# Kernel tuning notes

Measured on AMD Instinct MI355X. Metric: run time of the kernel, lower is better.

The kernel has to match this reference:

```python
import jax, jax.numpy as jnp
import numpy as np

B, S, E, H = 2, 2048, 512, 8
D = E // H
BETA = 0.5
SCALE = float(np.sqrt(D))


def setup_inputs() -> dict:
    key = jax.random.key(0)
    ks = jax.random.split(key, 22)
    inp = {}
    for i, n in enumerate(["qx", "qy", "kx", "ky", "vx", "vy"]):
        inp[n] = jax.random.normal(ks[i], (B, S, E), jnp.float32)
    wnames = ["Wqx", "Wqy", "Wkx", "Wky", "Wvx", "Wvy", "Wox", "Woy"]
    for i, n in enumerate(wnames):
        inp[n] = jax.random.normal(ks[6 + i], (E, E), jnp.float32) * 0.02
        inp["b" + n[1:]] = jnp.zeros((E,), jnp.float32)
    return inp


def _split_heads(x):
    # [B, S, E] -> [B, H, S, D]
    return x.reshape(B, S, H, D).transpose(0, 2, 1, 3)


def _merge_heads(x):
    # [B, H, S, D] -> [B, S, E]
    return x.transpose(0, 2, 1, 3).reshape(B, S, E)


def reference(qx, qy, kx, ky, vx, vy,
              Wqx, bqx, Wqy, bqy, Wkx, bkx, Wky, bky,
              Wvx, bvx, Wvy, bvy, Wox, box, Woy, boy):
    lin = lambda x, W, b: x @ W.T + b  # torch nn.Linear convention
    qxh = _split_heads(lin(qx, Wqx, bqx))
    qyh = _split_heads(lin(qy, Wqy, bqy))
    kxh = _split_heads(lin(kx, Wkx, bkx))
    kyh = _split_heads(lin(ky, Wky, bky))
    vxh = _split_heads(lin(vx, Wvx, bvx))
    vyh = _split_heads(lin(vy, Wvy, bvy))

    # polar decomposition of the bichannel: radius, angle
    aq = jnp.arctan2(qyh, qxh)  # [B,H,S,D]
    ak = jnp.arctan2(kyh, kxh)
    # mean_d cos(aq - ak) == (cos_q @ cos_k^T + sin_q @ sin_k^T) / D
    # (avoids the [B,H,Sq,Sk,D] angle_diff tensor; same math)
    phase = (jnp.einsum('bhqd,bhkd->bhqk', jnp.cos(aq), jnp.cos(ak))
             + jnp.einsum('bhqd,bhkd->bhqk', jnp.sin(aq), jnp.sin(ak))) / D

    rq = jnp.sqrt(qxh * qxh + qyh * qyh)
    rk = jnp.sqrt(kxh * kxh + kyh * kyh)
    mag = jnp.einsum('bhqd,bhkd->bhqk', rq, rk) / SCALE

    scores = BETA * phase + (1.0 - BETA) * mag  # [B,H,Sq,Sk]
    attn = jax.nn.softmax(scores, axis=-1)      # dropout is identity in eval

    ax = _merge_heads(jnp.einsum('bhqk,bhkd->bhqd', attn, vxh))
    ay = _merge_heads(jnp.einsum('bhqk,bhkd->bhqd', attn, vyh))
    return lin(ax, Wox, box), lin(ay, Woy, boy)
```

## Files before the change

kernel.cpp:

```cpp
#include <hip/hip_runtime.h>
#include <hip/hip_bf16.h>


#define N_ROWS 4096
#define EDIM 512
#define SEQ 2048
#define NHEAD 8
#define HDIM 64
#define CDIM 192
#define DV 128

#define PHASE_A 0.08838834764831845f
#define MAG_B   0.25f
#define SM_SHIFT 8.0f

typedef _Float16 half8 __attribute__((ext_vector_type(8)));
typedef float f32x4 __attribute__((ext_vector_type(4)));

__device__ inline void gload16(const void* g, void* l) {
    __builtin_amdgcn_global_load_lds(
        (const __attribute__((address_space(1))) unsigned int*)g,
        (__attribute__((address_space(3))) unsigned int*)l, 16, 0, 0);
}

#define KSW(r) (((((r) & 3) | (((r) >> 1) & 4))) << 4)

struct Cvt14 { const float* s[14]; _Float16* d[14]; int n8[14]; };

__global__ __launch_bounds__(256) void cvt_fp16(Cvt14 j) {
    const float* s = j.s[blockIdx.y];
    _Float16* d = j.d[blockIdx.y];
    const int n8 = j.n8[blockIdx.y];
    union U { _Float16 h[8]; uint4 u; };
    for (int i = blockIdx.x * 256 + threadIdx.x; i < n8; i += gridDim.x * 256) {
        const float4 f0 = ((const float4*)s)[2 * i];
        const float4 f1 = ((const float4*)s)[2 * i + 1];
        U u;
        u.h[0] = (_Float16)f0.x; u.h[1] = (_Float16)f0.y;
        u.h[2] = (_Float16)f0.z; u.h[3] = (_Float16)f0.w;
        u.h[4] = (_Float16)f1.x; u.h[5] = (_Float16)f1.y;
        u.h[6] = (_Float16)f1.z; u.h[7] = (_Float16)f1.w;
        ((uint4*)d)[i] = u.u;
    }
}

struct PairArgs {
    const _Float16* x0; const _Float16* x1;
    const _Float16* w0; const _Float16* w1;
    const float* b0;    const float* b1;
    void* dst0;         void* dst1;
};

template <int FUSED>
__global__ __launch_bounds__(256, 3) void gemm16(PairArgs A0, PairArgs A1, PairArgs A2)
{
    __shared__ _Float16 As0[128 * 32];
    __shared__ _Float16 As1[128 * 32];
    __shared__ _Float16 Bs0[64 * 32];
    __shared__ _Float16 Bs1[64 * 32];

    const int tid = threadIdx.x;
    const int w = tid >> 6, l = tid & 63;
    const int g = l >> 4, ql = l & 15;
    const int wr = w >> 1, wc = w & 1;
    const int z = FUSED ? blockIdx.z : 0;
    const PairArgs& A = FUSED ? (z == 0 ? A0 : (z == 1 ? A1 : A2)) : A0;

    const int m0 = blockIdx.y * 128;
    const int n0 = blockIdx.x * 64;

    f32x4 acc0[4][2], acc1[4][2];
    #pragma unroll
    for (int f = 0; f < 4; ++f)
        #pragma unroll
        for (int e = 0; e < 2; ++e) {
            acc0[f][e] = (f32x4){0.f, 0.f, 0.f, 0.f};
            acc1[f][e] = (f32x4){0.f, 0.f, 0.f, 0.f};
        }

    for (int k0 = 0; k0 < EDIM; k0 += 32) {
        __syncthreads();
        #pragma unroll
        for (int i = 0; i < 2; ++i) {
            const int s = i * 256 + tid;
            const int row = s >> 2, c = s & 3;
            const int cs = c ^ ((row >> 1) & 3);
            gload16(A.x0 + (size_t)(m0 + row) * EDIM + k0 + cs * 8,
                    As0 + (i * 256 + w * 64) * 8);
        }
        #pragma unroll
        for (int i = 0; i < 2; ++i) {
            const int s = i * 256 + tid;
            const int row = s >> 2, c = s & 3;
            const int cs = c ^ ((row >> 1) & 3);
            gload16(A.x1 + (size_t)(m0 + row) * EDIM + k0 + cs * 8,
                    As1 + (i * 256 + w * 64) * 8);
        }
        {
            const int row = tid >> 2, c = tid & 3;
            const int cs = c ^ ((row >> 1) & 3);
            gload16(A.w0 + (size_t)(n0 + row) * EDIM + k0 + cs * 8,
                    Bs0 + (w * 64) * 8);
            gload16(A.w1 + (size_t)(n0 + row) * EDIM + k0 + cs * 8,
                    Bs1 + (w * 64) * 8);
        }
        __syncthreads();

        half8 af0[4], af1[4], bf0[2], bf1[2];
        #pragma unroll
        for (int f = 0; f < 4; ++f) {
            const int arow = wr * 64 + f * 16 + ql;
            const int byo = arow * 64 + ((g ^ ((arow >> 1) & 3)) << 4);
            af0[f] = *(const half8*)((const char*)As0 + byo);
            af1[f] = *(const half8*)((const char*)As1 + byo);
        }
        #pragma unroll
        for (int e = 0; e < 2; ++e) {
            const int brow = wc * 32 + e * 16 + ql;
            const int byo = brow * 64 + ((g ^ ((brow >> 1) & 3)) << 4);
            bf0[e] = *(const half8*)((const char*)Bs0 + byo);
            bf1[e] = *(const half8*)((const char*)Bs1 + byo);
        }
        #pragma unroll
        for (int f = 0; f < 4; ++f)
            #pragma unroll
            for (int e = 0; e < 2; ++e) {
                acc0[f][e] = __builtin_amdgcn_mfma_f32_16x16x32_f16(
                    af0[f], bf0[e], acc0[f][e], 0, 0, 0);
                acc1[f][e] = __builtin_amdgcn_mfma_f32_16x16x32_f16(
                    af1[f], bf1[e], acc1[f][e], 0, 0, 0);
            }
    }

    #pragma unroll
    for (int f = 0; f < 4; ++f) {
        const int mb = m0 + wr * 64 + f * 16 + g * 4;
        #pragma unroll
        for (int e = 0; e < 2; ++e) {
            const int n = n0 + wc * 32 + e * 16 + ql;
            const float bias0 = A.b0[n];
            const float bias1 = A.b1[n];
            if (!FUSED) {
                float* o0 = (float*)A.dst0;
                float* o1 = (float*)A.dst1;
                #pragma unroll
                for (int r = 0; r < 4; ++r) {
                    const int m = mb + r;
                    o0[(size_t)m * EDIM + n] = acc0[f][e][r] + bias0;
                    o1[(size_t)m * EDIM + n] = acc1[f][e][r] + bias1;
                }
            } else {
                const int b = mb >> 11, s = mb & (SEQ - 1);
                const int h = blockIdx.x;
                const int d = n & (HDIM - 1);
                const int bh = b * NHEAD + h;
                _Float16* dst = (_Float16*)A.dst0;
                if (z != 2) {
                    const size_t base = ((size_t)bh * SEQ + s) * CDIM + d;
                    #pragma unroll
                    for (int r = 0; r < 4; ++r) {
                        const float v0 = acc0[f][e][r] + bias0;
                        const float v1 = acc1[f][e][r] + bias1;
                        const float r2 = v0 * v0 + v1 * v1;
                        const float rm = sqrtf(r2);
                        float c, sn;
                        if (r2 > 0.f) { c = v0 / rm; sn = v1 / rm; }
                        else          { c = 1.f;     sn = 0.f; }
                        dst[base + (size_t)r * CDIM]       = (_Float16)(c  * PHASE_A);
                        dst[base + (size_t)r * CDIM + 64]  = (_Float16)(sn * PHASE_A);
                        dst[base + (size_t)r * CDIM + 128] = (_Float16)(rm * MAG_B);
                    }
                } else {
                    union Pk { _Float16 h[4]; uint2 u; } p0, p1;
                    #pragma unroll
                    for (int r = 0; r < 4; ++r) {
                        p0.h[r] = (_Float16)(acc0[f][e][r] + bias0);
                        p1.h[r] = (_Float16)(acc1[f][e][r] + bias1);
                    }
                    *(uint2*)&dst[((size_t)bh * DV + d) * SEQ + s]      = p0.u;
                    *(uint2*)&dst[((size_t)bh * DV + 64 + d) * SEQ + s] = p1.u;
                }
            }
        }
    }
}

__global__ __launch_bounds__(512, 2) void attn_mfma(
    const _Float16* __restrict__ Qg, const _Float16* __restrict__ Kg,
    const _Float16* __restrict__ Vg,
    _Float16* __restrict__ ax, _Float16* __restrict__ ay)
{
    __shared__ char smem[81920];

    const int tid = threadIdx.x;
    const int w  = tid >> 6;
    const int l  = tid & 63;
    const int g  = l >> 4;
    const int ql = l & 15;

    const int d  = blockIdx.x;
    const int xcd = d & 7;
    const int j   = d >> 3;
    const int bh  = xcd + 8 * (j >> 4);
    const int q0  = (j & 15) * 128;
    const int b  = bh >> 3, h = bh & 7;
    const int qrow = q0 + w * 16 + ql;

    half8 qf[6];
    {
        const char* qp = (const char*)(Qg + ((size_t)bh * SEQ + qrow) * CDIM);
        #pragma unroll
        for (int c = 0; c < 6; ++c) {
            uint4 u = *(const uint4*)(qp + c * 64 + g * 16);
            qf[c] = __builtin_bit_cast(half8, u);
        }
    }

    f32x4 o[8];
    #pragma unroll
    for (int vt = 0; vt < 8; ++vt) o[vt] = (f32x4){0.f, 0.f, 0.f, 0.f};
    float l_i = 0.f;

    const char* kgb = (const char*)(Kg + (size_t)bh * SEQ * CDIM);
    const char* vgb = (const char*)(Vg + (size_t)bh * DV * SEQ);

    int koff[3], vofs[2];
    #pragma unroll
    for (int i = 0; i < 3; ++i) {
        const int beta = (w * 3 + i) * 1024 + l * 16;
        const int r = beta / 384;
        const int cb = (beta - r * 384) ^ KSW(r);
        koff[i] = r * 384 + cb;
    }
    #pragma unroll
    for (int i = 0; i < 2; ++i) {
        const int beta = (w * 2 + i) * 1024 + l * 16;
        const int r = beta >> 7;
        const int cb = (beta & 127) ^ ((r & 7) << 4);
        vofs[i] = r * 4096 + cb;
    }

    const int rq = ((ql >> 2) << 3) + (ql & 3);
    const int kxor = ((ql & 3) | (((ql >> 2) & 1) << 2)) << 4;

    #define STAGE(kbase, vbase, kt0)                                          \
        { _Pragma("unroll")                                                   \
          for (int i = 0; i < 3; ++i)                                         \
              gload16(kgb + (size_t)(kt0) * 384 + koff[i],                    \
                      smem + (kbase) + (w * 3 + i) * 1024);                   \
          _Pragma("unroll")                                                   \
          for (int i = 0; i < 2; ++i)                                         \
              gload16(vgb + (size_t)(kt0) * 2 + vofs[i],                      \
                      smem + (vbase) + (w * 2 + i) * 1024); }

    auto COMPUTE = [&](const int kbase, const int vbase) {
        f32x4 st[4];
        __builtin_amdgcn_s_setprio(1);
        #pragma unroll
        for (int kt = 0; kt < 4; ++kt) {
            f32x4 acc = {0.f, 0.f, 0.f, 0.f};
            const int r_p = rq + (kt & 1) * 32 + ((kt >> 1) << 2);
            #pragma unroll
            for (int c = 0; c < 6; ++c) {
                uint4 u = *(const uint4*)(
                    smem + kbase + ((r_p * 384 + c * 64 + g * 16) ^ kxor));
                acc = __builtin_amdgcn_mfma_f32_16x16x32_f16(
                    __builtin_bit_cast(half8, u), qf[c], acc, 0, 0, 0);
            }
            st[kt] = acc;
        }
        __builtin_amdgcn_s_setprio(0);

        float rs = 0.f;
        #pragma unroll
        for (int kt = 0; kt < 4; ++kt)
            #pragma unroll
            for (int r = 0; r < 4; ++r) {
                const float p = __expf(st[kt][r] - SM_SHIFT);
                st[kt][r] = p; rs += p;
            }
        rs += __shfl_xor(rs, 16);
        rs += __shfl_xor(rs, 32);
        l_i += rs;

        half8 pf[2];
        #pragma unroll
        for (int ks = 0; ks < 2; ++ks) {
            union { _Float16 h[8]; half8 v; } u;
            u.h[0] = (_Float16)st[ks][0];     u.h[1] = (_Float16)st[ks][1];
            u.h[2] = (_Float16)st[ks][2];     u.h[3] = (_Float16)st[ks][3];
            u.h[4] = (_Float16)st[ks + 2][0]; u.h[5] = (_Float16)st[ks + 2][1];
            u.h[6] = (_Float16)st[ks + 2][2]; u.h[7] = (_Float16)st[ks + 2][3];
            pf[ks] = u.v;
        }

        __builtin_amdgcn_s_setprio(1);
        #pragma unroll
        for (int vt = 0; vt < 8; ++vt) {
            const int v = vt * 16 + ql;
            uint4 u0 = *(const uint4*)(
                smem + vbase + ((v * 128 + g * 16) ^ ((v & 7) << 4)));
            uint4 u1 = *(const uint4*)(
                smem + vbase + ((v * 128 + 64 + g * 16) ^ ((v & 7) << 4)));
            o[vt] = __builtin_amdgcn_mfma_f32_16x16x32_f16(
                pf[0], __builtin_bit_cast(half8, u0), o[vt], 0, 0, 0);
            o[vt] = __builtin_amdgcn_mfma_f32_16x16x32_f16(
                pf[1], __builtin_bit_cast(half8, u1), o[vt], 0, 0, 0);
        }
        __builtin_amdgcn_s_setprio(0);
    };

    STAGE(0, 49152, 0);
    for (int t = 0; t < 32; t += 2) {
        __syncthreads();
        STAGE(24576, 65536, (t + 1) * 64);
        COMPUTE(0, 49152);
        __syncthreads();
        if (t + 2 < 32) STAGE(0, 49152, (t + 2) * 64);
        COMPUTE(24576, 65536);
    }
    #undef STAGE

    const float invl = 1.f / l_i;
    const float fi0 = __shfl(invl, g * 4 + 0);
    const float fi1 = __shfl(invl, g * 4 + 1);
    const float fi2 = __shfl(invl, g * 4 + 2);
    const float fi3 = __shfl(invl, g * 4 + 3);
    #pragma unroll
    for (int vt = 0; vt < 8; ++vt) {
        const int v = vt * 16 + ql;
        _Float16* basep = (vt < 4) ? ax : ay;
        const int vv = v & 63;
        const float fi[4] = {fi0, fi1, fi2, fi3};
        #pragma unroll
        for (int r = 0; r < 4; ++r) {
            const int q = q0 + w * 16 + g * 4 + r;
            basep[((size_t)(b * SEQ + q)) * EDIM + h * HDIM + vv] =
                (_Float16)(o[vt][r] * fi[r]);
        }
    }
}

extern "C" void kernel_launch(void* const* d_in, const int* in_sizes, int n_in,
                              void* d_out, int out_size, void* d_ws, size_t ws_size,
                              hipStream_t stream)
{
    const float* act[6];
    for (int i = 0; i < 6; ++i) act[i] = (const float*)d_in[i];
    const float* W[8]; const float* Bv[8];
    for (int i = 0; i < 8; ++i) {
        W[i]  = (const float*)d_in[6 + 2 * i];
        Bv[i] = (const float*)d_in[7 + 2 * i];
    }

    float* outx = (float*)d_out;
    float* outy = outx + 2097152;

    _Float16* ws = (_Float16*)d_ws;
    _Float16* act16[6];
    for (int i = 0; i < 6; ++i) act16[i] = ws + (size_t)i * 2097152;
    _Float16* w16[8];
    for (int i = 0; i < 8; ++i) w16[i] = ws + 12582912 + (size_t)i * 262144;
    _Float16* Qt16 = ws + 14680064;
    _Float16* Kt16 = Qt16 + 6291456;
    _Float16* Vt16 = Kt16 + 6291456;
    _Float16* ax16 = Vt16 + 4194304;
    _Float16* ay16 = ax16 + 2097152;

    Cvt14 jc{};
    for (int i = 0; i < 6; ++i) { jc.s[i] = act[i]; jc.d[i] = act16[i]; jc.n8[i] = 262144; }
    for (int i = 0; i < 8; ++i) { jc.s[6 + i] = W[i]; jc.d[6 + i] = w16[i]; jc.n8[6 + i] = 32768; }
    hipLaunchKernelGGL(cvt_fp16, dim3(256, 14), dim3(256), 0, stream, jc);

    PairArgs qa{act16[0], act16[1], w16[0], w16[1], Bv[0], Bv[1], Qt16, nullptr};
    PairArgs ka{act16[2], act16[3], w16[2], w16[3], Bv[2], Bv[3], Kt16, nullptr};
    PairArgs va{act16[4], act16[5], w16[4], w16[5], Bv[4], Bv[5], Vt16, nullptr};
    hipLaunchKernelGGL((gemm16<1>), dim3(8, 32, 3), dim3(256), 0, stream, qa, ka, va);

    hipLaunchKernelGGL(attn_mfma, dim3(256), dim3(512), 0, stream,
                       Qt16, Kt16, Vt16, ax16, ay16);

    PairArgs oa{ax16, ay16, w16[6], w16[7], Bv[6], Bv[7], outx, outy};
    hipLaunchKernelGGL((gemm16<0>), dim3(8, 32, 1), dim3(256), 0, stream, oa, oa, oa);
}
```

Before: 138.0 us.

## Fuse fp32-to-fp16 activation conversion into QKV GEMM and double-buffer LDS

Removes the separate conversion pass over the six fp32 activation tensors. The fused QKV GEMM now loads fp32 activations into registers, converts them to fp16 and writes them to LDS. The GEMM mainloop also becomes double-buffered, prefetching the next K slice while computing the current one, which takes one sync per iteration instead of two. This saves a full read and write of the activation traffic, but the GEMM now reads twice the bytes per activation tile and uses more registers and LDS, which may lower occupancy.

```diff
diff --git a/kernel.cpp b/kernel.cpp
--- a/kernel.cpp
+++ b/kernel.cpp
@@ -25,12 +25,11 @@
 
 #define KSW(r) (((((r) & 3) | (((r) >> 1) & 4))) << 4)
 
-struct Cvt14 { const float* s[14]; _Float16* d[14]; int n8[14]; };
-
-__global__ __launch_bounds__(256) void cvt_fp16(Cvt14 j) {
+struct Cvt8 { const float* s[8]; _Float16* d[8]; };
+
+__global__ __launch_bounds__(256) void cvt_fp16(Cvt8 j, int n8) {
     const float* s = j.s[blockIdx.y];
     _Float16* d = j.d[blockIdx.y];
-    const int n8 = j.n8[blockIdx.y];
     union U { _Float16 h[8]; uint4 u; };
     for (int i = blockIdx.x * 256 + threadIdx.x; i < n8; i += gridDim.x * 256) {
         const float4 f0 = ((const float4*)s)[2 * i];
@@ -45,7 +44,7 @@
 }
 
 struct PairArgs {
-    const _Float16* x0; const _Float16* x1;
+    const void* x0;     const void* x1;
     const _Float16* w0; const _Float16* w1;
     const float* b0;    const float* b1;
     void* dst0;         void* dst1;
@@ -54,10 +53,7 @@
 template <int FUSED>
 __global__ __launch_bounds__(256, 3) void gemm16(PairArgs A0, PairArgs A1, PairArgs A2)
 {
-    __shared__ _Float16 As0[128 * 32];
-    __shared__ _Float16 As1[128 * 32];
-    __shared__ _Float16 Bs0[64 * 32];
-    __shared__ _Float16 Bs1[64 * 32];
+    __shared__ _Float16 smem[2][12288];
 
     const int tid = threadIdx.x;
     const int w = tid >> 6, l = tid & 63;
@@ -69,6 +65,60 @@
     const int m0 = blockIdx.y * 128;
     const int n0 = blockIdx.x * 64;
 
+    size_t srcA[2];
+    #pragma unroll
+    for (int i = 0; i < 2; ++i) {
+        const int s = i * 256 + tid;
+        const int row = s >> 2, c = s & 3;
+        const int cs = c ^ ((row >> 1) & 3);
+        srcA[i] = (size_t)(m0 + row) * EDIM + cs * 8;
+    }
+    const int rowB = tid >> 2;
+    const int csB = (tid & 3) ^ ((rowB >> 1) & 3);
+    const size_t srcB = (size_t)(n0 + rowB) * EDIM + csB * 8;
+
+    const float* x0f = (const float*)A.x0;
+    const float* x1f = (const float*)A.x1;
+    const _Float16* x0h = (const _Float16*)A.x0;
+    const _Float16* x1h = (const _Float16*)A.x1;
+
+    float4 xr[2][2][2];
+
+    #define LOADX(k0)                                                         \
+        do { _Pragma("unroll")                                                \
+          for (int i = 0; i < 2; ++i) {                                       \
+              const float* p0 = x0f + srcA[i] + (k0);                         \
+              const float* p1 = x1f + srcA[i] + (k0);                         \
+              xr[0][i][0] = *(const float4*)p0;                               \
+              xr[0][i][1] = *(const float4*)(p0 + 4);                         \
+              xr[1][i][0] = *(const float4*)p1;                               \
+              xr[1][i][1] = *(const float4*)(p1 + 4);                         \
+          } } while (0)
+    #define WRITEX(buf)                                                       \
+        do { _Pragma("unroll")                                                \
+          for (int arr = 0; arr < 2; ++arr) {                                 \
+              _Pragma("unroll")                                               \
+              for (int i = 0; i < 2; ++i) {                                   \
+                  union { _Float16 h[8]; uint4 u; } t;                        \
+                  _Pragma("unroll")                                           \
+                  for (int jj = 0; jj < 4; ++jj) {                            \
+                      t.h[jj]     = (_Float16)xr[arr][i][0][jj];              \
+                      t.h[4 + jj] = (_Float16)xr[arr][i][1][jj];              \
+                  }                                                           \
+                  *(uint4*)&smem[buf][arr * 4096 + (i * 256 + tid) * 8] = t.u;\
+              } } } while (0)
+    #define STAGEX_LDS(buf, k0)                                               \
+        do { _Pragma("unroll")                                                \
+          for (int i = 0; i < 2; ++i) {                                       \
+              gload16(x0h + srcA[i] + (k0),                                   \
+                      &smem[buf][(i * 256 + w * 64) * 8]);                    \
+              gload16(x1h + srcA[i] + (k0),                                   \
+                      &smem[buf][4096 + (i * 256 + w * 64) * 8]);             \
+          } } while (0)
+    #define STAGEW(buf, k0)                                                   \
+        do { gload16(A.w0 + srcB + (k0), &smem[buf][8192 + w * 512]);         \
+             gload16(A.w1 + srcB + (k0), &smem[buf][10240 + w * 512]); } while (0)
+
     f32x4 acc0[4][2], acc1[4][2];
     #pragma unroll
     for (int f = 0; f < 4; ++f)
@@ -78,48 +128,21 @@
             acc1[f][e] = (f32x4){0.f, 0.f, 0.f, 0.f};
         }
 
-    for (int k0 = 0; k0 < EDIM; k0 += 32) {
-        __syncthreads();
-        #pragma unroll
-        for (int i = 0; i < 2; ++i) {
-            const int s = i * 256 + tid;
-            const int row = s >> 2, c = s & 3;
-            const int cs = c ^ ((row >> 1) & 3);
-            gload16(A.x0 + (size_t)(m0 + row) * EDIM + k0 + cs * 8,
-                    As0 + (i * 256 + w * 64) * 8);
-        }
-        #pragma unroll
-        for (int i = 0; i < 2; ++i) {
-            const int s = i * 256 + tid;
-            const int row = s >> 2, c = s & 3;
-            const int cs = c ^ ((row >> 1) & 3);
-            gload16(A.x1 + (size_t)(m0 + row) * EDIM + k0 + cs * 8,
-                    As1 + (i * 256 + w * 64) * 8);
-        }
-        {
-            const int row = tid >> 2, c = tid & 3;
-            const int cs = c ^ ((row >> 1) & 3);
-            gload16(A.w0 + (size_t)(n0 + row) * EDIM + k0 + cs * 8,
-                    Bs0 + (w * 64) * 8);
-            gload16(A.w1 + (size_t)(n0 + row) * EDIM + k0 + cs * 8,
-                    Bs1 + (w * 64) * 8);
-        }
-        __syncthreads();
-
+    auto COMPUTE = [&](int buf) {
         half8 af0[4], af1[4], bf0[2], bf1[2];
         #pragma unroll
         for (int f = 0; f < 4; ++f) {
             const int arow = wr * 64 + f * 16 + ql;
-            const int byo = arow * 64 + ((g ^ ((arow >> 1) & 3)) << 4);
-            af0[f] = *(const half8*)((const char*)As0 + byo);
-            af1[f] = *(const half8*)((const char*)As1 + byo);
+            const int ho = arow * 32 + (g ^ ((arow >> 1) & 3)) * 8;
+            af0[f] = *(const half8*)&smem[buf][ho];
+            af1[f] = *(const half8*)&smem[buf][4096 + ho];
         }
         #pragma unroll
         for (int e = 0; e < 2; ++e) {
             const int brow = wc * 32 + e * 16 + ql;
-            const int byo = brow * 64 + ((g ^ ((brow >> 1) & 3)) << 4);
-            bf0[e] = *(const half8*)((const char*)Bs0 + byo);
-            bf1[e] = *(const half8*)((const char*)Bs1 + byo);
+            const int ho = brow * 32 + (g ^ ((brow >> 1) & 3)) * 8;
+            bf0[e] = *(const half8*)&smem[buf][8192 + ho];
+            bf1[e] = *(const half8*)&smem[buf][10240 + ho];
         }
         #pragma unroll
         for (int f = 0; f < 4; ++f)
@@ -130,7 +153,37 @@
                 acc1[f][e] = __builtin_amdgcn_mfma_f32_16x16x32_f16(
                     af1[f], bf1[e], acc1[f][e], 0, 0, 0);
             }
-    }
+    };
+
+    if (FUSED) {
+        LOADX(0);
+        WRITEX(0);
+    } else {
+        STAGEX_LDS(0, 0);
+    }
+    STAGEW(0, 0);
+
+    for (int k0 = 0; k0 < EDIM; k0 += 32) {
+        const int cur = (k0 >> 5) & 1, nxt = cur ^ 1;
+        __syncthreads();
+        const bool more = (k0 + 32) < EDIM;
+        if (more) {
+            if (FUSED) {
+                LOADX(k0 + 32);
+            } else {
+                STAGEX_LDS(nxt, k0 + 32);
+            }
+            STAGEW(nxt, k0 + 32);
+        }
+        COMPUTE(cur);
+        if (more && FUSED) {
+            WRITEX(nxt);
+        }
+    }
+    #undef LOADX
+    #undef WRITEX
+    #undef STAGEX_LDS
+    #undef STAGEW
 
     #pragma unroll
     for (int f = 0; f < 4; ++f) {
@@ -244,14 +297,14 @@
     const int kxor = ((ql & 3) | (((ql >> 2) & 1) << 2)) << 4;
 
     #define STAGE(kbase, vbase, kt0)                                          \
-        { _Pragma("unroll")                                                   \
+        do { _Pragma("unroll")                                                \
           for (int i = 0; i < 3; ++i)                                         \
               gload16(kgb + (size_t)(kt0) * 384 + koff[i],                    \
                       smem + (kbase) + (w * 3 + i) * 1024);                   \
           _Pragma("unroll")                                                   \
           for (int i = 0; i < 2; ++i)                                         \
               gload16(vgb + (size_t)(kt0) * 2 + vofs[i],                      \
-                      smem + (vbase) + (w * 2 + i) * 1024); }
+                      smem + (vbase) + (w * 2 + i) * 1024); } while (0)
 
     auto COMPUTE = [&](const int kbase, const int vbase) {
         f32x4 st[4];
@@ -357,24 +410,21 @@
     float* outy = outx + 2097152;
 
     _Float16* ws = (_Float16*)d_ws;
-    _Float16* act16[6];
-    for (int i = 0; i < 6; ++i) act16[i] = ws + (size_t)i * 2097152;
     _Float16* w16[8];
-    for (int i = 0; i < 8; ++i) w16[i] = ws + 12582912 + (size_t)i * 262144;
-    _Float16* Qt16 = ws + 14680064;
+    for (int i = 0; i < 8; ++i) w16[i] = ws + (size_t)i * 262144;
+    _Float16* Qt16 = ws + 2097152;
     _Float16* Kt16 = Qt16 + 6291456;
     _Float16* Vt16 = Kt16 + 6291456;
     _Float16* ax16 = Vt16 + 4194304;
     _Float16* ay16 = ax16 + 2097152;
 
-    Cvt14 jc{};
-    for (int i = 0; i < 6; ++i) { jc.s[i] = act[i]; jc.d[i] = act16[i]; jc.n8[i] = 262144; }
-    for (int i = 0; i < 8; ++i) { jc.s[6 + i] = W[i]; jc.d[6 + i] = w16[i]; jc.n8[6 + i] = 32768; }
-    hipLaunchKernelGGL(cvt_fp16, dim3(256, 14), dim3(256), 0, stream, jc);
-
-    PairArgs qa{act16[0], act16[1], w16[0], w16[1], Bv[0], Bv[1], Qt16, nullptr};
-    PairArgs ka{act16[2], act16[3], w16[2], w16[3], Bv[2], Bv[3], Kt16, nullptr};
-    PairArgs va{act16[4], act16[5], w16[4], w16[5], Bv[4], Bv[5], Vt16, nullptr};
+    Cvt8 jw{};
+    for (int i = 0; i < 8; ++i) { jw.s[i] = W[i]; jw.d[i] = w16[i]; }
+    hipLaunchKernelGGL(cvt_fp16, dim3(128, 8), dim3(256), 0, stream, jw, 32768);
+
+    PairArgs qa{act[0], act[1], w16[0], w16[1], Bv[0], Bv[1], Qt16, nullptr};
+    PairArgs ka{act[2], act[3], w16[2], w16[3], Bv[2], Bv[3], Kt16, nullptr};
+    PairArgs va{act[4], act[5], w16[4], w16[5], Bv[4], Bv[5], Vt16, nullptr};
     hipLaunchKernelGGL((gemm16<1>), dim3(8, 32, 3), dim3(256), 0, stream, qa, ka, va);
 
     hipLaunchKernelGGL(attn_mfma, dim3(256), dim3(512), 0, stream,
```

Measured after the change: 146.6 us. 1.06x slower.
